# Kernel tuning notes

Measured on AMD Instinct MI355X. Metric: run time of the kernel, lower is better.

Reference implementation:

```python
import jax, jax.numpy as jnp
import numpy as np

N_HASHES = 4
CHUNK = 144
REDUCTION = 4

# PyTorch bicubic (a=-0.75), align_corners=False, integer scale 2 ->
# fixed fractional offsets t=0.75 (even outputs) and t=0.25 (odd outputs).
_EW = jnp.array([-0.03515625, 0.26171875, 0.87890625, -0.10546875], jnp.float32)
_OW = _EW[::-1]


def _up2_axis(x, axis):
    n = x.shape[axis]
    pad = [(0, 0)] * x.ndim
    pad[axis] = (2, 2)
    xp = jnp.pad(x, pad, mode='edge')  # torch clamps border indices
    sl = lambda s: jax.lax.slice_in_dim(xp, s, s + n, axis=axis)
    even = sum(_EW[k] * sl(k) for k in range(4))
    odd = sum(_OW[k] * sl(k + 1) for k in range(4))
    out = jnp.stack([even, odd], axis=axis + 1)
    shp = list(x.shape)
    shp[axis] = 2 * n
    return out.reshape(shp)


def bicubic_up2(x):
    return _up2_axis(_up2_axis(x, 2), 3)


def conv2d(x, w, b, pad):
    y = jax.lax.conv_general_dilated(x, w, (1, 1), [(pad, pad), (pad, pad)],
                                     dimension_numbers=('NCHW', 'OIHW', 'NCHW'))
    return y + b[None, :, None, None]


def _adj(t):
    # attend to own + two adjacent buckets along chunk axis (axis=2)
    return jnp.concatenate([t, jnp.roll(t, 1, axis=2), jnp.roll(t, -1, axis=2)], axis=3)


def nlsa(x, wm, bm, wa, ba, rot):
    N, Cc, H, W = x.shape
    L = H * W
    xe = conv2d(x, wm, bm, 1).reshape(N, -1, L).transpose(0, 2, 1)  # [N,L,C]
    ye = conv2d(x, wa, ba, 0).reshape(N, -1, L).transpose(0, 2, 1)  # [N,L,C*red]
    C = xe.shape[-1]
    hash_buckets = min(L // CHUNK + (L // CHUNK) % 2, 128)
    # LSH: random rotations -> argmax bucket codes (non-differentiable, detached)
    rotated = jnp.einsum('btf,fhi->bhti', xe, rot)  # [N,h,L,hb//2]
    rotated = jnp.concatenate([rotated, -rotated], axis=-1)  # [N,h,L,hb]
    codes = jnp.argmax(rotated, axis=-1)  # [N,h,L]
    codes = codes + (jnp.arange(N_HASHES) * hash_buckets)[None, :, None]
    codes = jax.lax.stop_gradient(codes.reshape(N, -1))  # [N,h*L]
    indices = jnp.argsort(codes, axis=-1)
    undo = jnp.argsort(indices, axis=-1)
    mod = indices % L
    xs = jnp.take_along_axis(xe, mod[..., None], axis=1)  # [N,h*L,C]
    ys = jnp.take_along_axis(ye, mod[..., None], axis=1)  # [N,h*L,C*red]
    padding = (-L) % CHUNK
    xb = xs.reshape(N, N_HASHES, L, C)
    yb = ys.reshape(N, N_HASHES, L, C * REDUCTION)
    if padding:
        xb = jnp.concatenate([xb, xb[:, :, -padding:, :]], axis=2)
        yb = jnp.concatenate([yb, yb[:, :, -padding:, :]], axis=2)
    nch = xb.shape[2] // CHUNK
    xb = xb.reshape(N, N_HASHES, nch, CHUNK, C)
    yb = yb.reshape(N, N_HASHES, nch, CHUNK, C * REDUCTION)
    xm = xb / jnp.maximum(jnp.linalg.norm(xb, axis=-1, keepdims=True), 5e-5)
    xm = _adj(xm)      # [N,h,k,3*chunk,C]
    ybj = _adj(yb)     # [N,h,k,3*chunk,C*red]
    raw = jnp.einsum('bhkie,bhkje->bhkij', xb, xm)  # [N,h,k,chunk,3*chunk]
    bscore = jax.scipy.special.logsumexp(raw, axis=-1, keepdims=True)
    score = jnp.exp(raw - bscore)
    ret = jnp.einsum('bhkij,bhkje->bhkie', score, ybj)
    ret = ret.reshape(N, N_HASHES, -1, C * REDUCTION)
    bscore = bscore.reshape(N, N_HASHES, -1)
    if padding:
        ret = ret[:, :, :-padding]
        bscore = bscore[:, :, :-padding]
    ret = ret.reshape(N, -1, C * REDUCTION)
    bscore = bscore.reshape(N, -1)
    ret = jnp.take_along_axis(ret, undo[..., None], axis=1)
    bscore = jnp.take_along_axis(bscore, undo, axis=1)
    ret = ret.reshape(N, N_HASHES, L, C * REDUCTION)
    probs = jax.nn.softmax(bscore.reshape(N, N_HASHES, L, 1), axis=1)
    ret = jnp.sum(ret * probs, axis=1)  # [N,L,C*red]
    return ret.transpose(0, 2, 1).reshape(N, -1, H, W) + x


def setup_inputs() -> dict:
    key = jax.random.key(0)
    ks = jax.random.split(key, 8)
    w = lambda k, shape, fan: (jax.random.normal(k, shape, jnp.float32) / np.sqrt(fan)).astype(jnp.float32)
    return {
        'x': jax.random.normal(ks[0], (2, 64, 96, 96), jnp.float32),
        'w1': w(ks[1], (64, 64, 3, 3), 64 * 9), 'b1': jnp.zeros((64,), jnp.float32),
        'w2': w(ks[2], (64, 64, 3, 3), 64 * 9), 'b2': jnp.zeros((64,), jnp.float32),
        'wm': w(ks[3], (16, 64, 3, 3), 64 * 9), 'bm': jnp.zeros((16,), jnp.float32),
        'wa': w(ks[4], (64, 64, 1, 1), 64), 'ba': jnp.zeros((64,), jnp.float32),
        'rot': jax.random.normal(ks[5], (16, N_HASHES, 64), jnp.float32),  # [C, h, hash_buckets//2]
    }


def reference(x, w1, b1, w2, b2, wm, bm, wa, ba, rot):
    x = bicubic_up2(x)
    x = jax.nn.relu(conv2d(x, w1, b1, 1))
    x = jax.nn.relu(conv2d(x, w2, b2, 1))
    return nlsa(x, wm, bm, wa, ba, rot)
```

## Files before the change

kernel.cpp:

```cpp
#include <hip/hip_runtime.h>
#include <math.h>

#define NB 2
#define CIN 64
#define H0 96
#define W0 96
#define HH 192
#define WW 192
#define LL (HH*WW)
#define NHASH 4
#define CHK 144
#define NCHK 256
#define CE 16
#define CV 64
#define NBUCK 128
#define SEGL 576
#define NSEG 64

#define K_ROWB   80
#define V_ROWB   912
#define P_ROWB   72
#define KQ_SZB   34560
#define VT_SZB   58368
#define PST_SZB  10368
#define LKI_SZB  1728
#define QN_SZB   576
#define LDS_T2   (KQ_SZB + VT_SZB + PST_SZB + LKI_SZB + QN_SZB)
#define LDS_T1   (VT_SZB + LKI_SZB)

typedef __attribute__((ext_vector_type(8))) short short8_t;
typedef __attribute__((ext_vector_type(4))) float f32x4;
union FragU { unsigned int u[4]; int4 i; short8_t s; };

__device__ __forceinline__ unsigned int cvtpk_bf16(float a, float b){
  unsigned int r;
  asm("v_cvt_pk_bf16_f32 %0, %1, %2" : "=v"(r) : "v"(a), "v"(b));
  return r;
}
__device__ __forceinline__ float bfl(unsigned int u){ return __uint_as_float(u << 16); }
__device__ __forceinline__ float bfh(unsigned int u){ return __uint_as_float(u & 0xffff0000u); }

__global__ __launch_bounds__(256) void k_upsample(const float* __restrict__ x,
                                                  float* __restrict__ out){
  int idx = blockIdx.x*256 + threadIdx.x;
  if (idx >= NB*CIN*HH*WW) return;
  int ox = idx % WW; int t2 = idx / WW;
  int oy = t2 % HH;  t2 /= HH;
  int i = oy >> 1, a = oy & 1;
  int j = ox >> 1, b = ox & 1;
  const float e0=-0.03515625f, e1=0.26171875f, e2=0.87890625f, e3=-0.10546875f;
  float wy[4], wx[4]; int ty[4], tx[4];
  if (a){ wy[0]=e3; wy[1]=e2; wy[2]=e1; wy[3]=e0; } else { wy[0]=e0; wy[1]=e1; wy[2]=e2; wy[3]=e3; }
  if (b){ wx[0]=e3; wx[1]=e2; wx[2]=e1; wx[3]=e0; } else { wx[0]=e0; wx[1]=e1; wx[2]=e2; wx[3]=e3; }
  int offy = a ? -1 : -2, offx = b ? -1 : -2;
  #pragma unroll
  for (int k=0;k<4;k++){
    int t = i + offy + k; ty[k] = t<0?0:(t>H0-1?H0-1:t);
    int s = j + offx + k; tx[k] = s<0?0:(s>W0-1?W0-1:s);
  }
  const float* xp = x + (size_t)t2*H0*W0;
  float s = 0.f;
  #pragma unroll
  for (int ky=0;ky<4;ky++){
    const float* row = xp + ty[ky]*W0;
    float rs = 0.f;
    rs = fmaf(wx[0], row[tx[0]], rs);
    rs = fmaf(wx[1], row[tx[1]], rs);
    rs = fmaf(wx[2], row[tx[2]], rs);
    rs = fmaf(wx[3], row[tx[3]], rs);
    s = fmaf(wy[ky], rs, s);
  }
  out[idx] = s;
}

__global__ __launch_bounds__(256) void k_prepw(const float* __restrict__ w,
    unsigned short* __restrict__ wsT, int CO){
  int idx = blockIdx.x*256 + threadIdx.x;
  if (idx >= CO*64*9) return;
  int tap = idx % 9; int rem = idx / 9;
  int ci = rem % 64; int co = rem / 64;
  float v = w[(size_t)(co*64 + ci)*9 + tap];
  unsigned int hu = cvtpk_bf16(v, v) & 0xffffu;
  float hf = bfl(hu);
  unsigned int lu = cvtpk_bf16(v - hf, 0.f) & 0xffffu;
  int half = ci >> 5, kg = (ci >> 3) & 3, e = ci & 7;
  size_t base = ((size_t)(tap*2 + half)*2)*CO*32 + ((size_t)co*4 + kg)*8 + e;
  wsT[base]         = (unsigned short)hu;
  wsT[base + (size_t)CO*32] = (unsigned short)lu;
}

template<int CO, bool RELU, bool OUT_NLC>
__global__ __launch_bounds__(256) void k_conv3m(const float* __restrict__ in,
    const unsigned short* __restrict__ wsT, const float* __restrict__ bias,
    float* __restrict__ out){
  __shared__ unsigned short inH[3][66][64];
  __shared__ unsigned short inL[3][66][64];
  const int t = threadIdx.x;
  const int bx = blockIdx.x, y = blockIdx.y, n = blockIdx.z;
  const int x0 = bx*64;
  const int l = t & 63, w = t >> 6;
  const int lq = l & 15, kg = l >> 4;

  for (int e = t; e < 3072; e += 256){
    const int chunk = e & 15;
    const int strip = e >> 4;
    const int ci = strip & 63, row = strip >> 6;
    const int gy = y + row - 1;
    float4 v = make_float4(0.f,0.f,0.f,0.f);
    if (gy >= 0 && gy < HH)
      v = *(const float4*)&in[(((size_t)n*CIN + ci)*HH + gy)*WW + x0 + chunk*4];
    float vv[4] = {v.x, v.y, v.z, v.w};
    #pragma unroll
    for (int j = 0; j < 4; ++j){
      const int col = 1 + chunk*4 + j;
      const int sci = (((ci >> 3) ^ (col & 7)) << 3) | (ci & 7);
      unsigned int hu = cvtpk_bf16(vv[j], vv[j]);
      unsigned int lu = cvtpk_bf16(vv[j] - bfl(hu), 0.f);
      inH[row][col][sci] = (unsigned short)hu;
      inL[row][col][sci] = (unsigned short)lu;
    }
  }
  if (t < 192){
    const int ci = t & 63, row = t >> 6;
    const int gy = y + row - 1;
    const bool okY = (gy >= 0 && gy < HH);
    const float* ip = &in[(((size_t)n*CIN + ci)*HH + (size_t)(okY?gy:0))*WW];
    float vL = (okY && x0 >= 1) ? ip[x0-1] : 0.f;
    float vR = (okY && x0+64 < WW) ? ip[x0+64] : 0.f;
    unsigned int hL = cvtpk_bf16(vL, vL);
    unsigned int lLu = cvtpk_bf16(vL - bfl(hL), 0.f);
    unsigned int hR = cvtpk_bf16(vR, vR);
    unsigned int lRu = cvtpk_bf16(vR - bfl(hR), 0.f);
    const int sci0 = ci;
    const int sci65 = (((ci >> 3) ^ 1) << 3) | (ci & 7);
    inH[row][0][sci0]  = (unsigned short)hL;  inL[row][0][sci0]  = (unsigned short)lLu;
    inH[row][65][sci65] = (unsigned short)hR; inL[row][65][sci65] = (unsigned short)lRu;
  }
  __syncthreads();

  constexpr int NCT = CO/16;
  f32x4 acc[NCT];
  #pragma unroll
  for (int c=0;c<NCT;c++) acc[c] = (f32x4){0.f,0.f,0.f,0.f};
  const unsigned short* wlane = wsT + (size_t)lq*32 + (size_t)kg*8;

  #pragma unroll
  for (int tap=0; tap<9; ++tap){
    const int ky = tap/3, kx = tap - ky*3;
    const int col = w*16 + lq + kx;
    #pragma unroll
    for (int half=0; half<2; ++half){
      const int sci = ((((half<<2) | kg) ^ (col & 7)) << 3);
      FragU Bh, Bl;
      Bh.i = *(const int4*)&inH[ky][col][sci];
      Bl.i = *(const int4*)&inL[ky][col][sci];
      const unsigned short* wth = wlane + (size_t)((tap*2+half)*2)*CO*32;
      #pragma unroll
      for (int ct=0; ct<NCT; ++ct){
        FragU Ah, Al;
        Ah.i = *(const int4*)(wth + ct*512);
        Al.i = *(const int4*)(wth + CO*32 + ct*512);
        acc[ct] = __builtin_amdgcn_mfma_f32_16x16x32_bf16(Ah.s, Bl.s, acc[ct], 0,0,0);
        acc[ct] = __builtin_amdgcn_mfma_f32_16x16x32_bf16(Al.s, Bh.s, acc[ct], 0,0,0);
        acc[ct] = __builtin_amdgcn_mfma_f32_16x16x32_bf16(Ah.s, Bh.s, acc[ct], 0,0,0);
      }
    }
  }

  const int px = x0 + w*16 + lq;
  if constexpr (!OUT_NLC){
    #pragma unroll
    for (int ct=0; ct<NCT; ++ct){
      #pragma unroll
      for (int r=0; r<4; ++r){
        const int co = ct*16 + kg*4 + r;
        float v = acc[ct][r] + bias[co];
        if (RELU) v = fmaxf(v, 0.f);
        out[(((size_t)n*CO + co)*HH + y)*WW + px] = v;
      }
    }
  } else {
    #pragma unroll
    for (int r=0; r<4; ++r){
      const int co = kg*4 + r;
      float v = acc[0][r] + bias[co];
      if (RELU) v = fmaxf(v, 0.f);
      out[((size_t)n*LL + y*WW + px)*CO + co] = v;
    }
  }
}

__global__ __launch_bounds__(256) void k_conv1x1(const float* __restrict__ x2,
    const float* __restrict__ wa, const float* __restrict__ ba,
    unsigned short* __restrict__ yeB){
  __shared__ float xs[64][64];
  __shared__ float wts[64][64];
  const int t = threadIdx.x;
  const int n = blockIdx.y;
  const int l0 = blockIdx.x*64;
  for (int e=t; e<4096; e+=256){
    int ci = e >> 6, l = e & 63;
    xs[ci][l]  = x2[((size_t)n*CIN+ci)*LL + l0 + l];
    wts[ci][l] = wa[(size_t)l*64 + ci];
  }
  __syncthreads();
  const int l = t & 63, cq = t >> 6;
  float acc[16];
  #pragma unroll
  for (int i=0;i<16;i++) acc[i] = ba[cq*16+i];
  for (int ci=0; ci<64; ci++){
    float xv = xs[ci][l];
    #pragma unroll
    for (int i=0;i<16;i++) acc[i] = fmaf(xv, wts[ci][cq*16+i], acc[i]);
  }
  unsigned int wds[8];
  #pragma unroll
  for (int i=0;i<8;i++) wds[i] = cvtpk_bf16(acc[2*i], acc[2*i+1]);
  uint4* op = (uint4*)&yeB[((size_t)n*LL + l0 + l)*64 + cq*16];
  op[0] = make_uint4(wds[0],wds[1],wds[2],wds[3]);
  op[1] = make_uint4(wds[4],wds[5],wds[6],wds[7]);
}

__global__ __launch_bounds__(128) void k_codes(const float* __restrict__ xe,
    const float* __restrict__ rot, unsigned char* __restrict__ codes){
  __shared__ float rs[NHASH][64][16];
  const int t = threadIdx.x;
  for (int e=t; e<4096; e+=128){
    int f = e >> 8; int rem = e & 255;
    int h = rem >> 6; int i = rem & 63;
    rs[h][i][f] = rot[((size_t)f*NHASH + h)*64 + i];
  }
  __syncthreads();
  const int n = blockIdx.y;
  const int l = blockIdx.x*128 + t;
  float q[16];
  const float* xr = &xe[((size_t)n*LL + l)*16];
  #pragma unroll
  for (int f=0;f<16;f++) q[f] = xr[f];
  #pragma unroll
  for (int h=0;h<NHASH;h++){
    float bp = -3.0e38f, bn = -3.0e38f; int ap=0, an=0;
    for (int i=0;i<64;i++){
      float s = 0.f;
      #pragma unroll
      for (int f=0;f<16;f++) s = fmaf(q[f], rs[h][i][f], s);
      if (s > bp){ bp = s; ap = i; }
      if (-s > bn){ bn = -s; an = i; }
    }
    int code = (bp >= bn) ? ap : (64 + an);
    codes[((size_t)n*NHASH + h)*LL + l] = (unsigned char)code;
  }
}

__global__ __launch_bounds__(256) void k_hist(const unsigned char* __restrict__ codes,
    unsigned int* __restrict__ segHist){
  __shared__ unsigned int h[NBUCK];
  const int t = threadIdx.x;
  if (t < NBUCK) h[t] = 0;
  __syncthreads();
  const int n = blockIdx.z, hh = blockIdx.y, s = blockIdx.x;
  const unsigned char* cp = codes + ((size_t)n*NHASH + hh)*LL + (size_t)s*SEGL;
  for (int e=t; e<SEGL; e+=256) atomicAdd(&h[cp[e]], 1u);
  __syncthreads();
  if (t < NBUCK)
    segHist[(((size_t)(n*NHASH+hh))*NSEG + s)*NBUCK + t] = h[t];
}

__global__ __launch_bounds__(128) void k_scan(unsigned int* __restrict__ segHist){
  __shared__ unsigned int tot[NBUCK];
  __shared__ unsigned int base[NBUCK];
  const int b = threadIdx.x;
  const size_t off = (size_t)blockIdx.x * NSEG * NBUCK;
  unsigned int run = 0;
  for (int s=0;s<NSEG;s++){
    unsigned int v = segHist[off + (size_t)s*NBUCK + b];
    segHist[off + (size_t)s*NBUCK + b] = run;
    run += v;
  }
  tot[b] = run;
  __syncthreads();
  if (b==0){ unsigned int r=0; for (int i=0;i<NBUCK;i++){ base[i]=r; r+=tot[i]; } }
  __syncthreads();
  const unsigned int bb = base[b];
  for (int s=0;s<NSEG;s++) segHist[off + (size_t)s*NBUCK + b] += bb;
}

__global__ __launch_bounds__(256) void k_rank(const unsigned char* __restrict__ codes,
    const unsigned int* __restrict__ segHist, int* __restrict__ srtIdx){
  __shared__ unsigned int cw[SEGL/4];
  __shared__ unsigned int sbase[NBUCK];
  const int t = threadIdx.x;
  const int n = blockIdx.z, hh = blockIdx.y, s = blockIdx.x;
  const size_t cb = ((size_t)n*NHASH + hh)*LL + (size_t)s*SEGL;
  const unsigned int* cp32 = (const unsigned int*)(codes + cb);
  for (int e=t; e<SEGL/4; e+=256) cw[e] = cp32[e];
  if (t < NBUCK)
    sbase[t] = segHist[(((size_t)(n*NHASH+hh))*NSEG + s)*NBUCK + t];
  __syncthreads();
  const size_t ob = ((size_t)n*NHASH + hh)*LL;
  for (int e=t; e<SEGL; e+=256){
    unsigned int c = (cw[e>>2] >> ((e&3)*8)) & 0xffu;
    unsigned int mul = c * 0x01010101u;
    int cnt = 0;
    const int nw = e >> 2;
    for (int wi=0; wi<nw; wi++){
      unsigned int v = cw[wi] ^ mul;
      unsigned int t1 = (v & 0x7f7f7f7fu) + 0x7f7f7f7fu;
      unsigned int z = ~(t1 | v) & 0x80808080u;
      cnt += __popc(z);
    }
    unsigned int lastw = cw[nw];
    const int nbp = e & 3;
    for (int bp=0; bp<nbp; bp++)
      if (((lastw >> (bp*8)) & 0xffu) == c) cnt++;
    int pos = (int)sbase[c] + cnt;
    srtIdx[ob + pos] = s*SEGL + e;
  }
}

__global__ __launch_bounds__(256) void k_gatherK(const float* __restrict__ xe,
    const int* __restrict__ srtIdx, unsigned short* __restrict__ Ksrt,
    float* __restrict__ normQ){
  const int idx = blockIdx.x*256 + threadIdx.x;
  if (idx >= NB*NHASH*LL) return;
  const int n = idx / (NHASH*LL);
  const int lk = srtIdx[idx];
  const float4* xr = (const float4*)&xe[((size_t)n*LL + lk)*16];
  float4 v0 = xr[0], v1 = xr[1], v2 = xr[2], v3 = xr[3];
  float f[16] = {v0.x,v0.y,v0.z,v0.w, v1.x,v1.y,v1.z,v1.w,
                 v2.x,v2.y,v2.z,v2.w, v3.x,v3.y,v3.z,v3.w};
  float ss = 0.f;
  #pragma unroll
  for (int i=0;i<16;i++) ss = fmaf(f[i], f[i], ss);
  const float nq = sqrtf(ss);
  normQ[idx] = nq;
  const float inv = 1.f / fmaxf(nq, 5e-5f);
  #pragma unroll
  for (int i=0;i<16;i++) f[i] *= inv;
  unsigned int kh[8], klo[8];
  #pragma unroll
  for (int i=0;i<8;i++) kh[i] = cvtpk_bf16(f[2*i], f[2*i+1]);
  #pragma unroll
  for (int i=0;i<8;i++)
    klo[i] = cvtpk_bf16(f[2*i] - bfl(kh[i]), f[2*i+1] - bfh(kh[i]));
  int4* kr = (int4*)(Ksrt + (size_t)idx*32);
  kr[0] = make_int4((int)kh[0],(int)kh[1],(int)kh[2],(int)kh[3]);
  kr[1] = make_int4((int)kh[4],(int)kh[5],(int)kh[6],(int)kh[7]);
  kr[2] = make_int4((int)klo[0],(int)klo[1],(int)klo[2],(int)klo[3]);
  kr[3] = make_int4((int)klo[4],(int)klo[5],(int)klo[6],(int)klo[7]);
}

__global__ __launch_bounds__(576) void k_attn4(const unsigned short* __restrict__ yeB,
    const int* __restrict__ srtIdx, const unsigned short* __restrict__ Ksrt,
    const float* __restrict__ normQ, unsigned short* __restrict__ retS,
    float* __restrict__ bscore){
  extern __shared__ char smem[];
  char* Vt  = smem;
  int* lkI  = (int*)(smem + VT_SZB);

  const int t = threadIdx.x;
  const int bx = blockIdx.x, hh = blockIdx.y, n = blockIdx.z;
  const int k = ((bx & 7) << 5) | (bx >> 3);
  const size_t sb = ((size_t)n*NHASH + hh)*LL;
  const int l = t & 63, w = t >> 6;
  const int lq16 = l & 15, g = l >> 4;

  if (t < 432){
    const int c3 = t / CHK, jl = t - c3*CHK;
    const int kc = (c3==0) ? k : ((c3==1) ? ((k+NCHK-1)&(NCHK-1)) : ((k+1)&(NCHK-1)));
    lkI[t] = srtIdx[sb + (size_t)kc*CHK + jl];
  }
  if (t < 512){
    int c = t >> 3, jp = t & 7;
    *(unsigned int*)(Vt + c*V_ROWB + 864 + jp*4) = 0u;
  }
  __syncthreads();

  #pragma unroll 4
  for (int it=0; it<24; ++it){
    const int e = t + it*576;
    const int jp = e >> 6, c = e & 63;
    const unsigned int a = yeB[((size_t)n*LL + lkI[2*jp  ])*64 + c];
    const unsigned int b = yeB[((size_t)n*LL + lkI[2*jp+1])*64 + c];
    *(unsigned int*)(Vt + c*V_ROWB + jp*4) = a | (b << 16);
  }
  const int qg = w*16 + lq16;
  const int pq = k*CHK + qg;
  const int lqs = lkI[qg];
  FragU b1, b2;
  const unsigned short* qrow = Ksrt + (sb + pq)*32;
  b1.i = *(const int4*)(qrow + (g&1)*8);
  if (g < 2) b2.i = *(const int4*)(qrow + 16 + (g&1)*8);
  else { b2.u[0]=0u; b2.u[1]=0u; b2.u[2]=0u; b2.u[3]=0u; }
  const float nq_ = normQ[sb + pq];
  const float msc = fmaxf(nq_, 5e-5f);
  __syncthreads();

  const int sl0 = lq16 + ((g & 1) << 5);
  const int sl1 = sl0 + 16;
  const bool loTile = (g < 2);

  float sum = 0.f;
  f32x4 O0 = {0.f,0.f,0.f,0.f}, O1 = O0, O2 = O0, O3 = O0;

  for (int u=0; u<14; ++u){
    unsigned int pk[2][2];
    #pragma unroll
    for (int sub=0; sub<2; ++sub){
      const int t27 = 2*u + sub;
      if (t27 < 27){
        const int c3 = t27 / 9;
        const int kc = (c3==0) ? k : ((c3==1) ? ((k+NCHK-1)&(NCHK-1)) : ((k+1)&(NCHK-1)));
        const int row16 = (t27 - c3*9)*16;
        FragU a; a.i = *(const int4*)(Ksrt + (sb + (size_t)kc*CHK + row16 + lq16)*32 + g*8);
        f32x4 C = {0.f,0.f,0.f,0.f};
        C = __builtin_amdgcn_mfma_f32_16x16x32_bf16(a.s, b2.s, C, 0, 0, 0);
        C = __builtin_amdgcn_mfma_f32_16x16x32_bf16(a.s, b1.s, C, 0, 0, 0);
        const float p0 = __expf(fmaf(msc, C[0], -nq_));
        const float p1 = __expf(fmaf(msc, C[1], -nq_));
        const float p2 = __expf(fmaf(msc, C[2], -nq_));
        const float p3 = __expf(fmaf(msc, C[3], -nq_));
        sum += (p0+p1) + (p2+p3);
        pk[sub][0] = cvtpk_bf16(p0, p1);
        pk[sub][1] = cvtpk_bf16(p2, p3);
      } else {
        pk[sub][0] = 0u; pk[sub][1] = 0u;
      }
    }
    const unsigned int a00 = __shfl(pk[0][0], sl0), a01 = __shfl(pk[0][1], sl0);
    const unsigned int a10 = __shfl(pk[1][0], sl0), a11 = __shfl(pk[1][1], sl0);
    const unsigned int b00 = __shfl(pk[0][0], sl1), b01 = __shfl(pk[0][1], sl1);
    const unsigned int b10 = __shfl(pk[1][0], sl1), b11 = __shfl(pk[1][1], sl1);
    FragU bp;
    bp.u[0] = loTile ? a00 : a10;
    bp.u[1] = loTile ? a01 : a11;
    bp.u[2] = loTile ? b00 : b10;
    bp.u[3] = loTile ? b01 : b11;

    const char* Vb = Vt + lq16*V_ROWB + u*64 + g*16;
    FragU av0, av1, av2, av3;
    av0.i = *(const int4*)(Vb);
    av1.i = *(const int4*)(Vb + 16*V_ROWB);
    av2.i = *(const int4*)(Vb + 32*V_ROWB);
    av3.i = *(const int4*)(Vb + 48*V_ROWB);
    O0 = __builtin_amdgcn_mfma_f32_16x16x32_bf16(av0.s, bp.s, O0, 0,0,0);
    O1 = __builtin_amdgcn_mfma_f32_16x16x32_bf16(av1.s, bp.s, O1, 0,0,0);
    O2 = __builtin_amdgcn_mfma_f32_16x16x32_bf16(av2.s, bp.s, O2, 0,0,0);
    O3 = __builtin_amdgcn_mfma_f32_16x16x32_bf16(av3.s, bp.s, O3, 0,0,0);
  }
  sum += __shfl_xor(sum, 16);
  sum += __shfl_xor(sum, 32);
  const float linv = 1.f / sum;

  unsigned short* op = &retS[(sb + lqs)*64];
  {
    uint2 s0 = make_uint2(cvtpk_bf16(O0[0]*linv, O0[1]*linv), cvtpk_bf16(O0[2]*linv, O0[3]*linv));
    uint2 s1 = make_uint2(cvtpk_bf16(O1[0]*linv, O1[1]*linv), cvtpk_bf16(O1[2]*linv, O1[3]*linv));
    uint2 s2 = make_uint2(cvtpk_bf16(O2[0]*linv, O2[1]*linv), cvtpk_bf16(O2[2]*linv, O2[3]*linv));
    uint2 s3 = make_uint2(cvtpk_bf16(O3[0]*linv, O3[1]*linv), cvtpk_bf16(O3[2]*linv, O3[3]*linv));
    *(uint2*)(op +  0 + g*4) = s0;
    *(uint2*)(op + 16 + g*4) = s1;
    *(uint2*)(op + 32 + g*4) = s2;
    *(uint2*)(op + 48 + g*4) = s3;
  }
  if (g == 0) bscore[sb + lqs] = nq_ + logf(sum);
}

__global__ __launch_bounds__(576) void k_attn2b(const float* __restrict__ xe,
    const unsigned short* __restrict__ yeB, const int* __restrict__ srtIdx,
    unsigned short* __restrict__ retS, float* __restrict__ bscore){
  extern __shared__ char smem[];
  unsigned short* Kq = (unsigned short*)smem;
  char* Vt  = smem + KQ_SZB;
  char* Pst = Vt + VT_SZB;
  int* lkI  = (int*)(Pst + PST_SZB);
  float* qn = (float*)(Pst + PST_SZB + LKI_SZB);

  const int t = threadIdx.x;
  const int bx = blockIdx.x, hh = blockIdx.y, n = blockIdx.z;
  const int k = ((bx & 7) << 5) | (bx >> 3);
  const size_t sb = ((size_t)n*NHASH + hh)*LL;
  const int l = t & 63, w = t >> 6;
  const int lq16 = l & 15, g = l >> 4;

  if (t < 432){
    const int c3 = t / CHK, jl = t - c3*CHK;
    const int kc = (c3==0) ? k : ((c3==1) ? ((k+NCHK-1)&(NCHK-1)) : ((k+1)&(NCHK-1)));
    const int lk = srtIdx[sb + (size_t)kc*CHK + jl];
    lkI[t] = lk;
    const float4* xr = (const float4*)&xe[((size_t)n*LL + lk)*16];
    float4 v0 = xr[0], v1 = xr[1], v2 = xr[2], v3 = xr[3];
    float f[16] = {v0.x,v0.y,v0.z,v0.w, v1.x,v1.y,v1.z,v1.w,
                   v2.x,v2.y,v2.z,v2.w, v3.x,v3.y,v3.z,v3.w};
    float ss = 0.f;
    #pragma unroll
    for (int i=0;i<16;i++) ss = fmaf(f[i], f[i], ss);
    const float nq = sqrtf(ss);
    if (c3 == 0) qn[jl] = nq;
    const float inv = 1.f / fmaxf(nq, 5e-5f);
    #pragma unroll
    for (int i=0;i<16;i++) f[i] *= inv;
    unsigned int kh[8], klo[8];
    #pragma unroll
    for (int i=0;i<8;i++) kh[i] = cvtpk_bf16(f[2*i], f[2*i+1]);
    #pragma unroll
    for (int i=0;i<8;i++)
      klo[i] = cvtpk_bf16(f[2*i] - bfl(kh[i]), f[2*i+1] - bfh(kh[i]));
    int4* kr = (int4*)((char*)Kq + t*K_ROWB);
    kr[0] = make_int4((int)kh[0],(int)kh[1],(int)kh[2],(int)kh[3]);
    kr[1] = make_int4((int)kh[4],(int)kh[5],(int)kh[6],(int)kh[7]);
    kr[2] = make_int4((int)klo[0],(int)klo[1],(int)klo[2],(int)klo[3]);
    kr[3] = make_int4((int)klo[4],(int)klo[5],(int)klo[6],(int)klo[7]);
  }
  if (t < 512){
    int c = t >> 3, jp = t & 7;
    *(unsigned int*)(Vt + c*V_ROWB + 864 + jp*4) = 0u;
  }
  __syncthreads();

  #pragma unroll 4
  for (int it=0; it<24; ++it){
    const int e = t + it*576;
    const int jp = e >> 6, c = e & 63;
    const unsigned int a = yeB[((size_t)n*LL + lkI[2*jp  ])*64 + c];
    const unsigned int b = yeB[((size_t)n*LL + lkI[2*jp+1])*64 + c];
    *(unsigned int*)(Vt + c*V_ROWB + jp*4) = a | (b << 16);
  }
  const int qg = w*16 + lq16;
  const int lqs = lkI[qg];
  FragU b1, b2;
  float nq_;
  {
    const char* qrow = (const char*)Kq + qg*K_ROWB;
    b1.i = *(const int4*)(qrow + (g&1)*16);
    if (g < 2) b2.i = *(const int4*)(qrow + 32 + (g&1)*16);
    else { b2.u[0]=0u; b2.u[1]=0u; b2.u[2]=0u; b2.u[3]=0u; }
    nq_ = qn[qg];
  }
  const float msc = fmaxf(nq_, 5e-5f);
  __syncthreads();

  float sum = 0.f;
  f32x4 O0 = {0.f,0.f,0.f,0.f}, O1 = O0, O2 = O0, O3 = O0;
  char* Pw = Pst + w*(16*P_ROWB);
  for (int u=0; u<14; ++u){
    #pragma unroll
    for (int sub=0; sub<2; ++sub){
      const int t27 = u*2 + sub;
      uint2 pw;
      if (t27 < 27){
        FragU a;
        a.i = *(const int4*)((const char*)Kq + (size_t)(t27*16 + lq16)*K_ROWB + g*16);
        f32x4 C = {0.f,0.f,0.f,0.f};
        C = __builtin_amdgcn_mfma_f32_16x16x32_bf16(a.s, b2.s, C, 0, 0, 0);
        C = __builtin_amdgcn_mfma_f32_16x16x32_bf16(a.s, b1.s, C, 0, 0, 0);
        const float p0 = __expf(fmaf(msc, C[0], -nq_));
        const float p1 = __expf(fmaf(msc, C[1], -nq_));
        const float p2 = __expf(fmaf(msc, C[2], -nq_));
        const float p3 = __expf(fmaf(msc, C[3], -nq_));
        sum += (p0+p1) + (p2+p3);
        pw = make_uint2(cvtpk_bf16(p0,p1), cvtpk_bf16(p2,p3));
      } else {
        pw = make_uint2(0u, 0u);
      }
      *(uint2*)(Pw + lq16*P_ROWB + sub*32 + g*8) = pw;
    }
    asm volatile("s_waitcnt lgkmcnt(0)" ::: "memory");
    __builtin_amdgcn_sched_barrier(0);
    FragU bp; bp.i = *(const int4*)(Pw + lq16*P_ROWB + g*16);
    const char* Vb = Vt + lq16*V_ROWB + u*64 + g*16;
    FragU av;
    av.i = *(const int4*)(Vb);             O0 = __builtin_amdgcn_mfma_f32_16x16x32_bf16(av.s, bp.s, O0, 0,0,0);
    av.i = *(const int4*)(Vb + 16*V_ROWB); O1 = __builtin_amdgcn_mfma_f32_16x16x32_bf16(av.s, bp.s, O1, 0,0,0);
    av.i = *(const int4*)(Vb + 32*V_ROWB); O2 = __builtin_amdgcn_mfma_f32_16x16x32_bf16(av.s, bp.s, O2, 0,0,0);
    av.i = *(const int4*)(Vb + 48*V_ROWB); O3 = __builtin_amdgcn_mfma_f32_16x16x32_bf16(av.s, bp.s, O3, 0,0,0);
  }
  sum += __shfl_xor(sum, 16);
  sum += __shfl_xor(sum, 32);
  const float linv = 1.f / sum;

  unsigned short* op = &retS[(sb + lqs)*64];
  {
    uint2 s0 = make_uint2(cvtpk_bf16(O0[0]*linv, O0[1]*linv), cvtpk_bf16(O0[2]*linv, O0[3]*linv));
    uint2 s1 = make_uint2(cvtpk_bf16(O1[0]*linv, O1[1]*linv), cvtpk_bf16(O1[2]*linv, O1[3]*linv));
    uint2 s2 = make_uint2(cvtpk_bf16(O2[0]*linv, O2[1]*linv), cvtpk_bf16(O2[2]*linv, O2[3]*linv));
    uint2 s3 = make_uint2(cvtpk_bf16(O3[0]*linv, O3[1]*linv), cvtpk_bf16(O3[2]*linv, O3[3]*linv));
    *(uint2*)(op +  0 + g*4) = s0;
    *(uint2*)(op + 16 + g*4) = s1;
    *(uint2*)(op + 32 + g*4) = s2;
    *(uint2*)(op + 48 + g*4) = s3;
  }
  if (g == 0) bscore[sb + lqs] = nq_ + logf(sum);
}

__global__ __launch_bounds__(256) void k_combine(const unsigned short* __restrict__ retS,
    const float* __restrict__ bscore, const float* __restrict__ x2,
    float* __restrict__ out){
  const int idx = blockIdx.x*256 + threadIdx.x;
  if (idx >= NB*LL) return;
  const int l = idx % LL, n = idx / LL;
  float bs[NHASH];
  #pragma unroll
  for (int h=0;h<NHASH;h++)
    bs[h] = bscore[((size_t)n*NHASH + h)*LL + l];
  float m = fmaxf(fmaxf(bs[0],bs[1]), fmaxf(bs[2],bs[3]));
  float wsum = 0.f; float wv[NHASH];
  #pragma unroll
  for (int h=0;h<NHASH;h++){ wv[h] = expf(bs[h]-m); wsum += wv[h]; }
  const float winv = 1.f / wsum;
  float o[64];
  #pragma unroll
  for (int i=0;i<64;i++) o[i]=0.f;
  #pragma unroll
  for (int h=0;h<NHASH;h++){
    const float wh = wv[h]*winv;
    const uint4* rp = (const uint4*)&retS[(((size_t)n*NHASH + h)*LL + l)*64];
    #pragma unroll
    for (int i2=0;i2<8;i2++){
      uint4 v = rp[i2];
      o[i2*8+0] = fmaf(wh, bfl(v.x), o[i2*8+0]);
      o[i2*8+1] = fmaf(wh, bfh(v.x), o[i2*8+1]);
      o[i2*8+2] = fmaf(wh, bfl(v.y), o[i2*8+2]);
      o[i2*8+3] = fmaf(wh, bfh(v.y), o[i2*8+3]);
      o[i2*8+4] = fmaf(wh, bfl(v.z), o[i2*8+4]);
      o[i2*8+5] = fmaf(wh, bfh(v.z), o[i2*8+5]);
      o[i2*8+6] = fmaf(wh, bfl(v.w), o[i2*8+6]);
      o[i2*8+7] = fmaf(wh, bfh(v.w), o[i2*8+7]);
    }
  }
  #pragma unroll
  for (int c=0;c<64;c++){
    size_t oi = ((size_t)n*64 + c)*LL + l;
    out[oi] = o[c] + x2[oi];
  }
}

extern "C" void kernel_launch(void* const* d_in, const int* in_sizes, int n_in,
                              void* d_out, int out_size, void* d_ws, size_t ws_size,
                              hipStream_t stream){
  const float* x   = (const float*)d_in[0];
  const float* w1  = (const float*)d_in[1];
  const float* b1  = (const float*)d_in[2];
  const float* w2  = (const float*)d_in[3];
  const float* b2  = (const float*)d_in[4];
  const float* wm  = (const float*)d_in[5];
  const float* bm  = (const float*)d_in[6];
  const float* wa  = (const float*)d_in[7];
  const float* ba  = (const float*)d_in[8];
  const float* rot = (const float*)d_in[9];
  float* outp = (float*)d_out;
  char* ws = (char*)d_ws;
  const size_t FM   = (size_t)NB*CIN*HH*WW*sizeof(float);
  const size_t YEB  = (size_t)NB*LL*64*2;
  const size_t RETB = (size_t)NB*NHASH*LL*64*2;
  const size_t NHL4 = (size_t)NB*NHASH*LL*4;

  char* p = ws;
  unsigned short* yeB = (unsigned short*)p;  p += YEB;
  char* regA = p;                            p += RETB;
  float* x2  = (float*)p;                    p += FM;
  float* xe  = (float*)p;                    p += (size_t)NB*LL*CE*sizeof(float);
  unsigned char* codes = (unsigned char*)p;  p += (size_t)NB*NHASH*LL;
  unsigned int* segHist = (unsigned int*)p;  p += (size_t)NB*NHASH*NSEG*NBUCK*4;
  int* srtIdx  = (int*)p;                    p += NHL4;
  float* bscore = (float*)p;                 p += NHL4;
  unsigned short* wsT1 = (unsigned short*)p; p += (size_t)9*2*2*64*32*2;
  unsigned short* wsT2 = (unsigned short*)p; p += (size_t)9*2*2*64*32*2;
  unsigned short* wsTm = (unsigned short*)p; p += (size_t)9*2*2*16*32*2;
  const size_t needT2 = (size_t)(p - ws);
  unsigned short* Ksrt = (unsigned short*)p; p += (size_t)NB*NHASH*LL*32*2;
  float* normQ = (float*)p;                  p += NHL4;
  const size_t needT1 = (size_t)(p - ws);

  unsigned short* retS = (unsigned short*)regA;
  float* x0u = (float*)regA;
  float* y1  = (float*)(regA + FM);
  if (ws_size < needT2) return;
  const bool preg = (ws_size >= needT1);

  hipFuncSetAttribute((const void*)k_attn4,
                      hipFuncAttributeMaxDynamicSharedMemorySize, LDS_T1);
  hipFuncSetAttribute((const void*)k_attn2b,
                      hipFuncAttributeMaxDynamicSharedMemorySize, LDS_T2);

  k_prepw<<<dim3((64*64*9+255)/256), dim3(256), 0, stream>>>(w1, wsT1, 64);
  k_prepw<<<dim3((64*64*9+255)/256), dim3(256), 0, stream>>>(w2, wsT2, 64);
  k_prepw<<<dim3((16*64*9+255)/256), dim3(256), 0, stream>>>(wm, wsTm, 16);
  k_upsample<<<dim3((NB*CIN*HH*WW+255)/256), dim3(256), 0, stream>>>(x, x0u);
  k_conv3m<64,true,false><<<dim3(3, HH, NB), dim3(256), 0, stream>>>(x0u, wsT1, b1, y1);
  k_conv3m<64,true,false><<<dim3(3, HH, NB), dim3(256), 0, stream>>>(y1, wsT2, b2, x2);
  k_conv3m<16,false,true><<<dim3(3, HH, NB), dim3(256), 0, stream>>>(x2, wsTm, bm, xe);
  k_conv1x1<<<dim3(LL/64, NB), dim3(256), 0, stream>>>(x2, wa, ba, yeB);
  k_codes<<<dim3(LL/128, NB), dim3(128), 0, stream>>>(xe, rot, codes);
  k_hist<<<dim3(NSEG, NHASH, NB), dim3(256), 0, stream>>>(codes, segHist);
  k_scan<<<dim3(NB*NHASH), dim3(128), 0, stream>>>(segHist);
  k_rank<<<dim3(NSEG, NHASH, NB), dim3(256), 0, stream>>>(codes, segHist, srtIdx);
  if (preg){
    k_gatherK<<<dim3((NB*NHASH*LL+255)/256), dim3(256), 0, stream>>>(xe, srtIdx, Ksrt, normQ);
    k_attn4<<<dim3(NCHK, NHASH, NB), dim3(576), LDS_T1, stream>>>(
        yeB, srtIdx, Ksrt, normQ, retS, bscore);
  } else {
    k_attn2b<<<dim3(NCHK, NHASH, NB), dim3(576), LDS_T2, stream>>>(
        xe, yeB, srtIdx, retS, bscore);
  }
  k_combine<<<dim3((NB*LL+255)/256), dim3(256), 0, stream>>>(retS, bscore, x2, outp);
}
```

Before: 366.3 us.

## Software-pipeline QK scores through per-wave LDS staging in attention kernel

Rewrites the attention inner loop so the QK MFMA and exp for step u+1 overlap the PV MFMAs of step u, with K fragments prefetched two tiles ahead. The cross-lane shuffle that rebuilt the probability fragment is replaced by a per-wave LDS staging buffer, which adds LDS usage and an explicit lgkmcnt wait each iteration. The swizzled chunk-to-block mapping is also dropped in favour of a linear blockIdx mapping in both attention kernels. The larger LDS footprint may lower occupancy, and the LDS round trip adds latency that the overlap is meant to hide.

```diff
diff --git a/kernel.cpp b/kernel.cpp
--- a/kernel.cpp
+++ b/kernel.cpp
@@ -26,7 +26,7 @@
 #define LKI_SZB  1728
 #define QN_SZB   576
 #define LDS_T2   (KQ_SZB + VT_SZB + PST_SZB + LKI_SZB + QN_SZB)
-#define LDS_T1   (VT_SZB + LKI_SZB)
+#define LDS_T1   (VT_SZB + PST_SZB + LKI_SZB)
 
 typedef __attribute__((ext_vector_type(8))) short short8_t;
 typedef __attribute__((ext_vector_type(4))) float f32x4;
@@ -350,17 +350,17 @@
   kr[3] = make_int4((int)klo[4],(int)klo[5],(int)klo[6],(int)klo[7]);
 }
 
-__global__ __launch_bounds__(576) void k_attn4(const unsigned short* __restrict__ yeB,
+__global__ __launch_bounds__(576) void k_attn5(const unsigned short* __restrict__ yeB,
     const int* __restrict__ srtIdx, const unsigned short* __restrict__ Ksrt,
     const float* __restrict__ normQ, unsigned short* __restrict__ retS,
     float* __restrict__ bscore){
   extern __shared__ char smem[];
   char* Vt  = smem;
-  int* lkI  = (int*)(smem + VT_SZB);
+  char* Pst = smem + VT_SZB;
+  int* lkI  = (int*)(Pst + PST_SZB);
 
   const int t = threadIdx.x;
-  const int bx = blockIdx.x, hh = blockIdx.y, n = blockIdx.z;
-  const int k = ((bx & 7) << 5) | (bx >> 3);
+  const int k = blockIdx.x, hh = blockIdx.y, n = blockIdx.z;
   const size_t sb = ((size_t)n*NHASH + hh)*LL;
   const int l = t & 63, w = t >> 6;
   const int lq16 = l & 15, g = l >> 4;
@@ -396,57 +396,83 @@
   const float msc = fmaxf(nq_, 5e-5f);
   __syncthreads();
 
-  const int sl0 = lq16 + ((g & 1) << 5);
-  const int sl1 = sl0 + 16;
-  const bool loTile = (g < 2);
-
+  char* const Pw = Pst + w*(16*P_ROWB);
+  const int pwr = lq16*P_ROWB;
   float sum = 0.f;
   f32x4 O0 = {0.f,0.f,0.f,0.f}, O1 = O0, O2 = O0, O3 = O0;
 
+  auto kaddr = [&](int t27)->const int4*{
+    const int c3 = t27 / 9;
+    const int kc = (c3==0) ? k : ((c3==1) ? ((k+NCHK-1)&(NCHK-1)) : ((k+1)&(NCHK-1)));
+    const int row16 = (t27 - c3*9)*16;
+    return (const int4*)(Ksrt + (sb + (size_t)kc*CHK + row16 + lq16)*32 + g*8);
+  };
+
+  FragU aC0, aC1;
+  aC0.i = *kaddr(0);
+  aC1.i = *kaddr(1);
+  #pragma unroll
+  for (int sub=0; sub<2; ++sub){
+    FragU a = (sub==0) ? aC0 : aC1;
+    f32x4 C = {0.f,0.f,0.f,0.f};
+    C = __builtin_amdgcn_mfma_f32_16x16x32_bf16(a.s, b2.s, C, 0, 0, 0);
+    C = __builtin_amdgcn_mfma_f32_16x16x32_bf16(a.s, b1.s, C, 0, 0, 0);
+    const float p0 = __expf(fmaf(msc, C[0], -nq_));
+    const float p1 = __expf(fmaf(msc, C[1], -nq_));
+    const float p2 = __expf(fmaf(msc, C[2], -nq_));
+    const float p3 = __expf(fmaf(msc, C[3], -nq_));
+    sum += (p0+p1) + (p2+p3);
+    *(uint2*)(Pw + pwr + sub*32 + g*8) = make_uint2(cvtpk_bf16(p0,p1), cvtpk_bf16(p2,p3));
+  }
+  aC0.i = *kaddr(2);
+  aC1.i = *kaddr(3);
+
   for (int u=0; u<14; ++u){
-    unsigned int pk[2][2];
-    #pragma unroll
-    for (int sub=0; sub<2; ++sub){
-      const int t27 = 2*u + sub;
-      if (t27 < 27){
-        const int c3 = t27 / 9;
-        const int kc = (c3==0) ? k : ((c3==1) ? ((k+NCHK-1)&(NCHK-1)) : ((k+1)&(NCHK-1)));
-        const int row16 = (t27 - c3*9)*16;
-        FragU a; a.i = *(const int4*)(Ksrt + (sb + (size_t)kc*CHK + row16 + lq16)*32 + g*8);
-        f32x4 C = {0.f,0.f,0.f,0.f};
-        C = __builtin_amdgcn_mfma_f32_16x16x32_bf16(a.s, b2.s, C, 0, 0, 0);
-        C = __builtin_amdgcn_mfma_f32_16x16x32_bf16(a.s, b1.s, C, 0, 0, 0);
-        const float p0 = __expf(fmaf(msc, C[0], -nq_));
-        const float p1 = __expf(fmaf(msc, C[1], -nq_));
-        const float p2 = __expf(fmaf(msc, C[2], -nq_));
-        const float p3 = __expf(fmaf(msc, C[3], -nq_));
-        sum += (p0+p1) + (p2+p3);
-        pk[sub][0] = cvtpk_bf16(p0, p1);
-        pk[sub][1] = cvtpk_bf16(p2, p3);
-      } else {
-        pk[sub][0] = 0u; pk[sub][1] = 0u;
-      }
-    }
-    const unsigned int a00 = __shfl(pk[0][0], sl0), a01 = __shfl(pk[0][1], sl0);
-    const unsigned int a10 = __shfl(pk[1][0], sl0), a11 = __shfl(pk[1][1], sl0);
-    const unsigned int b00 = __shfl(pk[0][0], sl1), b01 = __shfl(pk[0][1], sl1);
-    const unsigned int b10 = __shfl(pk[1][0], sl1), b11 = __shfl(pk[1][1], sl1);
-    FragU bp;
-    bp.u[0] = loTile ? a00 : a10;
-    bp.u[1] = loTile ? a01 : a11;
-    bp.u[2] = loTile ? b00 : b10;
-    bp.u[3] = loTile ? b01 : b11;
-
+    asm volatile("s_waitcnt lgkmcnt(0)" ::: "memory");
+    __builtin_amdgcn_sched_barrier(0);
+    FragU bp; bp.i = *(const int4*)(Pw + pwr + g*16);
     const char* Vb = Vt + lq16*V_ROWB + u*64 + g*16;
     FragU av0, av1, av2, av3;
     av0.i = *(const int4*)(Vb);
     av1.i = *(const int4*)(Vb + 16*V_ROWB);
     av2.i = *(const int4*)(Vb + 32*V_ROWB);
     av3.i = *(const int4*)(Vb + 48*V_ROWB);
+    const FragU aT0 = aC0, aT1 = aC1;
+    if (u < 12){
+      aC0.i = *kaddr(2*u+4);
+      if (2*u+5 < 27) aC1.i = *kaddr(2*u+5);
+    }
+    unsigned int pkw[4];
+    const bool doQK = (u < 13);
+    if (doQK){
+      #pragma unroll
+      for (int sub=0; sub<2; ++sub){
+        const int t27 = 2*(u+1) + sub;
+        if (t27 < 27){
+          FragU a = (sub==0) ? aT0 : aT1;
+          f32x4 C = {0.f,0.f,0.f,0.f};
+          C = __builtin_amdgcn_mfma_f32_16x16x32_bf16(a.s, b2.s, C, 0, 0, 0);
+          C = __builtin_amdgcn_mfma_f32_16x16x32_bf16(a.s, b1.s, C, 0, 0, 0);
+          const float p0 = __expf(fmaf(msc, C[0], -nq_));
+          const float p1 = __expf(fmaf(msc, C[1], -nq_));
+          const float p2 = __expf(fmaf(msc, C[2], -nq_));
+          const float p3 = __expf(fmaf(msc, C[3], -nq_));
+          sum += (p0+p1) + (p2+p3);
+          pkw[sub*2+0] = cvtpk_bf16(p0, p1);
+          pkw[sub*2+1] = cvtpk_bf16(p2, p3);
+        } else {
+          pkw[sub*2+0] = 0u; pkw[sub*2+1] = 0u;
+        }
+      }
+    }
     O0 = __builtin_amdgcn_mfma_f32_16x16x32_bf16(av0.s, bp.s, O0, 0,0,0);
     O1 = __builtin_amdgcn_mfma_f32_16x16x32_bf16(av1.s, bp.s, O1, 0,0,0);
     O2 = __builtin_amdgcn_mfma_f32_16x16x32_bf16(av2.s, bp.s, O2, 0,0,0);
     O3 = __builtin_amdgcn_mfma_f32_16x16x32_bf16(av3.s, bp.s, O3, 0,0,0);
+    if (doQK){
+      *(uint2*)(Pw + pwr + 0*32 + g*8) = make_uint2(pkw[0], pkw[1]);
+      *(uint2*)(Pw + pwr + 1*32 + g*8) = make_uint2(pkw[2], pkw[3]);
+    }
   }
   sum += __shfl_xor(sum, 16);
   sum += __shfl_xor(sum, 32);
@@ -477,8 +503,7 @@
   float* qn = (float*)(Pst + PST_SZB + LKI_SZB);
 
   const int t = threadIdx.x;
-  const int bx = blockIdx.x, hh = blockIdx.y, n = blockIdx.z;
-  const int k = ((bx & 7) << 5) | (bx >> 3);
+  const int k = blockIdx.x, hh = blockIdx.y, n = blockIdx.z;
   const size_t sb = ((size_t)n*NHASH + hh)*LL;
   const int l = t & 63, w = t >> 6;
   const int lq16 = l & 15, g = l >> 4;
@@ -678,7 +703,7 @@
   if (ws_size < needT2) return;
   const bool preg = (ws_size >= needT1);
 
-  hipFuncSetAttribute((const void*)k_attn4,
+  hipFuncSetAttribute((const void*)k_attn5,
                       hipFuncAttributeMaxDynamicSharedMemorySize, LDS_T1);
   hipFuncSetAttribute((const void*)k_attn2b,
                       hipFuncAttributeMaxDynamicSharedMemorySize, LDS_T2);
@@ -697,7 +722,7 @@
   k_rank<<<dim3(NSEG, NHASH, NB), dim3(256), 0, stream>>>(codes, segHist, srtIdx);
   if (preg){
     k_gatherK<<<dim3((NB*NHASH*LL+255)/256), dim3(256), 0, stream>>>(xe, srtIdx, Ksrt, normQ);
-    k_attn4<<<dim3(NCHK, NHASH, NB), dim3(576), LDS_T1, stream>>>(
+    k_attn5<<<dim3(NCHK, NHASH, NB), dim3(576), LDS_T1, stream>>>(
         yeB, srtIdx, Ksrt, normQ, retS, bscore);
   } else {
     k_attn2b<<<dim3(NCHK, NHASH, NB), dim3(576), LDS_T2, stream>>>(
```

New measurement: 370.1 us. No clear change (+1.0%).
